# Kernel optimization log

Hardware: AMD Instinct MI355X
Metric: run time of the kernel (lower is better)

Reference implementation:

```python
import jax, jax.numpy as jnp
import numpy as np
from jax import lax

BN_EPS = 1e-5

def _conv1d_same(x, w):
    # x: [N, 1, C], w: [1, 1, k] with k odd -> SAME padding along channel axis
    k = w.shape[-1]
    return lax.conv_general_dilated(x, w, window_strides=(1,),
                                    padding=[(k // 2, k // 2)],
                                    dimension_numbers=('NCH', 'OIH', 'NCH'))

def setup_inputs() -> dict:
    key = jax.random.key(0)
    ks = jax.random.split(key, 6)
    B, C, H, W = 4, 64, 64, 64
    kk = 3  # kernel size from in_dim=64: t=int(abs(log2(64)+1)/2)=3 (odd)
    x = jax.random.normal(ks[0], (B, C, H, W), dtype=jnp.float32)
    q_w = jax.random.normal(ks[1], (1, 1, kk), dtype=jnp.float32) * 0.5
    k_w = jax.random.normal(ks[2], (1, 1, kk), dtype=jnp.float32) * 0.5
    v_w = jax.random.normal(ks[3], (C, C), dtype=jnp.float32) * (1.0 / np.sqrt(C))
    v_b = jnp.zeros((C,), dtype=jnp.float32)
    gamma = jax.random.uniform(ks[4], (1,), dtype=jnp.float32, minval=0.5, maxval=1.5)
    bn_w = jnp.ones((C,), dtype=jnp.float32)
    bn_b = jnp.zeros((C,), dtype=jnp.float32)
    return {"x": x, "q_w": q_w, "k_w": k_w, "v_w": v_w, "v_b": v_b,
            "gamma": gamma, "bn_w": bn_w, "bn_b": bn_b}

def reference(x, q_w, k_w, v_w, v_b, gamma, bn_w, bn_b):
    B, C, H, W = x.shape
    N = H * W
    # conv1d Q/K projections over the channel axis, per spatial position
    xp = x.reshape(B, C, N).transpose(0, 2, 1).reshape(B * N, 1, C)
    q = _conv1d_same(xp, q_w).reshape(B, N, C)   # proj_query: [B, HW, C]
    k = _conv1d_same(xp, k_w).reshape(B, N, C)   # proj_key (pre-permute)
    energy = jnp.einsum('bnc,bmc->bnm', q, k)    # [B, HW, HW]
    attn = jax.nn.softmax(energy, axis=-1)
    # 1x1 value conv
    v = jnp.einsum('oc,bchw->bohw', v_w, x) + v_b[None, :, None, None]
    vv = v.reshape(B, C, N)
    # bmm(value, attention^T)
    out = jnp.einsum('bcm,bnm->bcn', vv, attn).reshape(B, C, H, W)
    y = gamma[0] * out
    # BatchNorm2d, training mode (batch statistics, biased variance)
    mean = jnp.mean(y, axis=(0, 2, 3), keepdims=True)
    var = jnp.var(y, axis=(0, 2, 3), keepdims=True)
    y = (y - mean) * lax.rsqrt(var + BN_EPS)
    y = y * bn_w[None, :, None, None] + bn_b[None, :, None, None]
    return y + x
```

## Files before the change

### kernel.cpp

```cpp
#include <hip/hip_runtime.h>
#include <stdint.h>

using f16 = _Float16;

typedef _Float16 f16x8 __attribute__((ext_vector_type(8)));
typedef _Float16 f16x4 __attribute__((ext_vector_type(4)));
typedef float f32x4 __attribute__((ext_vector_type(4)));

#define LOG2E 1.44269504088896340736f

__device__ __forceinline__ f16 f2h(float f) { return (f16)f; }

#if __has_builtin(__builtin_amdgcn_exp2f)
__device__ __forceinline__ float fexp2(float x) { return __builtin_amdgcn_exp2f(x); }
#else
__device__ __forceinline__ float fexp2(float x) { return exp2f(x); }
#endif

typedef __attribute__((address_space(1))) const uint32_t gu32;
typedef __attribute__((address_space(3))) uint32_t lu32;

__device__ __forceinline__ void dma16(const void* g, void* l) {
  __builtin_amdgcn_global_load_lds((gu32*)g, (lu32*)l, 16, 0, 0);
}

__device__ __forceinline__ f16x8 cvt8(const float* p) {
  const float4 a = *(const float4*)p;
  const float4 b = *(const float4*)(p + 4);
  f16x8 r;
  r[0] = (f16)a.x; r[1] = (f16)a.y; r[2] = (f16)a.z; r[3] = (f16)a.w;
  r[4] = (f16)b.x; r[5] = (f16)b.y; r[6] = (f16)b.z; r[7] = (f16)b.w;
  return r;
}


__global__ __launch_bounds__(256, 2) void pam_pre(
    const float* __restrict__ x, const float* __restrict__ qw,
    const float* __restrict__ kw, const float* __restrict__ vw,
    const float* __restrict__ vb,
    f16* __restrict__ qa, f16* __restrict__ ka2, f16* __restrict__ va3,
    float* __restrict__ gz)
{
  __shared__ alignas(16) f16 xt[16 * 72];
  const int tid = threadIdx.x;
  const int b = blockIdx.x >> 8;
  const int n0 = (blockIdx.x & 255) << 4;
  const int lane = tid & 63;
  const int wv = tid >> 6;
  const int quad = lane >> 4, l15 = lane & 15;

  if (blockIdx.x == 0 && tid < 128) gz[tid] = 0.f;

  {
    const int c = tid >> 2;
    const int j0 = (tid & 3) << 2;
    const float4 v0 = *(const float4*)(x + ((size_t)(b * 64 + c) << 12) + n0 + j0);
    xt[(j0 + 0) * 72 + c] = f2h(v0.x);
    xt[(j0 + 1) * 72 + c] = f2h(v0.y);
    xt[(j0 + 2) * 72 + c] = f2h(v0.z);
    xt[(j0 + 3) * 72 + c] = f2h(v0.w);
  }
  __syncthreads();

  if (tid < 128) {
    const float qw0 = qw[0], qw1 = qw[1], qw2 = qw[2];
    const float kw0 = kw[0], kw1 = kw[1], kw2 = kw[2];
    const int n = tid >> 3;
    const int c8 = tid & 7;
    const f16x8 v0 = *(const f16x8*)&xt[n * 72 + c8 * 8];
    const float lm = (c8 > 0) ? (float)xt[n * 72 + c8 * 8 - 1] : 0.f;
    const float rp = (c8 < 7) ? (float)xt[n * 72 + c8 * 8 + 8] : 0.f;
    f16x8 qv8, kv8;
#pragma unroll
    for (int j = 0; j < 8; ++j) {
      const float xm = (j == 0) ? lm : (float)v0[j - 1];
      const float x0 = (float)v0[j];
      const float xp = (j == 7) ? rp : (float)v0[j + 1];
      qv8[j] = f2h((qw0 * xm + qw1 * x0 + qw2 * xp) * LOG2E);
      kv8[j] = f2h(kw0 * xm + kw1 * x0 + kw2 * xp);
    }
    const int nn = n0 + n;
    *(f16x8*)(qa + ((size_t)((b << 12) + nn) << 6) + c8 * 8) = qv8;
    const int np = nn ^ ((((nn >> 3) & 1) << 2) | ((nn >> 4) & 1));
    *(f16x8*)(ka2 + (((size_t)(b * 8 + c8)) << 15) + (np << 3)) = kv8;
  }

  {
    const f16x8 a0 = *(const f16x8*)&xt[l15 * 72 + quad * 8];
    const f16x8 a1 = *(const f16x8*)&xt[l15 * 72 + quad * 8 + 32];
    const int co = wv * 16 + l15;
    const f16x8 b0 = cvt8(vw + co * 64 + quad * 8);
    const f16x8 b1 = cvt8(vw + co * 64 + quad * 8 + 32);
    f32x4 z = {0.f, 0.f, 0.f, 0.f};
    z = __builtin_amdgcn_mfma_f32_16x16x32_f16(a0, b0, z, 0, 0, 0);
    z = __builtin_amdgcn_mfma_f32_16x16x32_f16(a1, b1, z, 0, 0, 0);
    const float vbv = vb[co];
    f16x4 pv;
#pragma unroll
    for (int r = 0; r < 4; ++r) pv[r] = f2h(z[r] + vbv);
    const int nb = n0 + quad * 4;
    *(f16x4*)(va3 + (((size_t)(b * 512 + (nb >> 3))) << 9)
              + (co << 3) + (nb & 7)) = pv;
  }
}

__global__ __launch_bounds__(512, 6) void pam_attn(
    const f16* __restrict__ qa, const f16* __restrict__ ka2,
    const f16* __restrict__ va3, const float* __restrict__ gam,
    float* __restrict__ y0, float* __restrict__ gs1, float* __restrict__ gs2)
{
  __shared__ alignas(16) f16 kbuf[2][8192];
  __shared__ float ldsO[32 * 65];
  __shared__ float ldsM[4][32], ldsL[4][32], ldsMg[32], ldsInv[32];

  const int tid = threadIdx.x;
  const int wv = tid >> 6, lane = tid & 63;
  const int quad = lane >> 4, l15 = lane & 15;
  const int ks = wv & 3, qh = wv >> 2;
  const int b = blockIdx.x & 3;
  const int qb = blockIdx.x >> 2;
  const int qb0 = qb << 5;
  const int phase = qb & 31;

  for (int i = tid; i < 32 * 65; i += 512) ldsO[i] = 0.f;

  const int bn = b << 12;
  f16x8 bq0, bq1;
  {
    const int q = qb0 + qh * 16 + l15;
    const f16* qp = qa + ((size_t)(bn + q) << 6) + quad * 8;
    bq0 = *(const f16x8*)qp;
    bq1 = *(const f16x8*)(qp + 32);
  }

  const f16* kg0 = ka2 + (((size_t)(b * 8 + wv)) << 15) + (lane << 3);
  const f16* vgp = va3 + ((size_t)b << 18) + ((ks * 4 + quad) << 9) + (l15 << 3);

  f32x4 o[4] = {};
  float m = -1e30f, lp = 0.f;

  dma16(kg0 + ((size_t)phase << 10),       kbuf[0] + (wv << 10));
  dma16(kg0 + ((size_t)phase << 10) + 512, kbuf[0] + (wv << 10) + 512);
  __syncthreads();

  const int u = l15 >> 2;
  const int xmsk = ((u & 1) << 2) | (u >> 1);
  const int pos0 = (ks << 5) + (u << 3) + (l15 & 3);
  const int koff0 = (pos0 ^ xmsk) << 3;
  const int koff1 = koff0 ^ 32;

#pragma unroll 1
  for (int kt = 0; kt < 32; ++kt) {
    const int cur = kt & 1;
    const int gcur = (kt + phase) & 31;

    const f16* vt = vgp + ((size_t)gcur << 13);
    const f16x8 av0 = *(const f16x8*)(vt);
    const f16x8 av1 = *(const f16x8*)(vt + 128);
    const f16x8 av2 = *(const f16x8*)(vt + 256);
    const f16x8 av3 = *(const f16x8*)(vt + 384);

    {
      const int tn = (kt + 1 + phase) & 31;
      f16* kd = kbuf[cur ^ 1] + (wv << 10);
      dma16(kg0 + ((size_t)tn << 10),       kd);
      dma16(kg0 + ((size_t)tn << 10) + 512, kd + 512);
    }

    const f16* kc = kbuf[cur];
    const f16x8 ak00 = *(const f16x8*)(kc + (quad << 10) + koff0);
    const f16x8 ak01 = *(const f16x8*)(kc + ((4 + quad) << 10) + koff0);
    const f16x8 ak10 = *(const f16x8*)(kc + (quad << 10) + koff1);
    const f16x8 ak11 = *(const f16x8*)(kc + ((4 + quad) << 10) + koff1);

    f32x4 z0, z1;
    {
      f32x4 z = {0.f, 0.f, 0.f, 0.f};
      z = __builtin_amdgcn_mfma_f32_16x16x32_f16(ak00, bq0, z, 0, 0, 0);
      z0 = __builtin_amdgcn_mfma_f32_16x16x32_f16(ak01, bq1, z, 0, 0, 0);
    }
    {
      f32x4 z = {0.f, 0.f, 0.f, 0.f};
      z = __builtin_amdgcn_mfma_f32_16x16x32_f16(ak10, bq0, z, 0, 0, 0);
      z1 = __builtin_amdgcn_mfma_f32_16x16x32_f16(ak11, bq1, z, 0, 0, 0);
    }

    float tmax = fmaxf(fmaxf(fmaxf(z0[0], z0[1]), fmaxf(z0[2], z0[3])),
                       fmaxf(fmaxf(z1[0], z1[1]), fmaxf(z1[2], z1[3])));
    tmax = fmaxf(tmax, __shfl_xor(tmax, 16, 64));
    tmax = fmaxf(tmax, __shfl_xor(tmax, 32, 64));
    const bool need = !__all(tmax <= m + 8.f);
    const float mn = need ? fmaxf(m, tmax) : m;

    const float p0 = fexp2(z0[0] - mn);
    const float p1 = fexp2(z0[1] - mn);
    const float p2 = fexp2(z0[2] - mn);
    const float p3 = fexp2(z0[3] - mn);
    const float p4 = fexp2(z1[0] - mn);
    const float p5 = fexp2(z1[1] - mn);
    const float p6 = fexp2(z1[2] - mn);
    const float p7 = fexp2(z1[3] - mn);
    const float ts = ((p0 + p1) + (p2 + p3)) + ((p4 + p5) + (p6 + p7));

    f16x8 pa;
    pa[0] = f2h(p0); pa[1] = f2h(p1); pa[2] = f2h(p2); pa[3] = f2h(p3);
    pa[4] = f2h(p4); pa[5] = f2h(p5); pa[6] = f2h(p6); pa[7] = f2h(p7);

    if (need) {
      const float al = fexp2(m - mn);
      lp = lp * al + ts;
      m = mn;
#pragma unroll
      for (int ct = 0; ct < 4; ++ct)
        for (int r = 0; r < 4; ++r) o[ct][r] *= al;
    } else {
      lp += ts;
    }

    o[0] = __builtin_amdgcn_mfma_f32_16x16x32_f16(av0, pa, o[0], 0, 0, 0);
    o[1] = __builtin_amdgcn_mfma_f32_16x16x32_f16(av1, pa, o[1], 0, 0, 0);
    o[2] = __builtin_amdgcn_mfma_f32_16x16x32_f16(av2, pa, o[2], 0, 0, 0);
    o[3] = __builtin_amdgcn_mfma_f32_16x16x32_f16(av3, pa, o[3], 0, 0, 0);
    __syncthreads();
  }

  {
    float v = lp;
    v += __shfl_xor(v, 16, 64);
    v += __shfl_xor(v, 32, 64);
    if (quad == 0) {
      ldsM[ks][qh * 16 + l15] = m;
      ldsL[ks][qh * 16 + l15] = v;
    }
  }
  __syncthreads();

  if (tid < 32) {
    const float M = fmaxf(fmaxf(ldsM[0][tid], ldsM[1][tid]),
                          fmaxf(ldsM[2][tid], ldsM[3][tid]));
    const float lt = ldsL[0][tid] * fexp2(ldsM[0][tid] - M) +
                     ldsL[1][tid] * fexp2(ldsM[1][tid] - M) +
                     ldsL[2][tid] * fexp2(ldsM[2][tid] - M) +
                     ldsL[3][tid] * fexp2(ldsM[3][tid] - M);
    ldsMg[tid] = M;
    ldsInv[tid] = 1.f / lt;
  }
  __syncthreads();

  {
    const int q = qh * 16 + l15;
    const float sc = fexp2(m - ldsMg[q]);
#pragma unroll
    for (int ct = 0; ct < 4; ++ct)
      for (int r = 0; r < 4; ++r)
        atomicAdd(&ldsO[q * 65 + ct * 16 + quad * 4 + r], o[ct][r] * sc);
  }
  __syncthreads();

  const float g = gam[0];
  {
    const int c = tid >> 3;
    const int q0 = (tid & 7) << 2;
    float4 v4;
    float* vp = &v4.x;
    float s1 = 0.f, s2 = 0.f;
    for (int r = 0; r < 4; ++r) {
      const float val = g * ldsO[(q0 + r) * 65 + c] * ldsInv[q0 + r];
      vp[r] = val; s1 += val; s2 += val * val;
    }
    *(float4*)(y0 + ((size_t)(b * 64 + c) << 12) + qb0 + q0) = v4;
    s1 += __shfl_xor(s1, 1, 64);
    s2 += __shfl_xor(s2, 1, 64);
    s1 += __shfl_xor(s1, 2, 64);
    s2 += __shfl_xor(s2, 2, 64);
    s1 += __shfl_xor(s1, 4, 64);
    s2 += __shfl_xor(s2, 4, 64);
    if ((tid & 7) == 0) {
      atomicAdd(&gs1[c], s1);
      atomicAdd(&gs2[c], s2);
    }
  }
}

__global__ __launch_bounds__(256, 2) void pam_apply(
    const float* __restrict__ y0, const float* __restrict__ x,
    const float* __restrict__ gs1, const float* __restrict__ gs2,
    const float* __restrict__ bnw, const float* __restrict__ bnb,
    float* __restrict__ out)
{
  const int i = (blockIdx.x * 256 + threadIdx.x) << 2;
  const int c = (i >> 12) & 63;
  const float inv_n = 1.f / 16384.f;
  const float mean = gs1[c] * inv_n;
  const float var = fmaxf(gs2[c] * inv_n - mean * mean, 0.f);
  const float sc = bnw[c] * rsqrtf(var + 1e-5f);
  const float sh = bnb[c] - mean * sc;
  const float4 y = *(const float4*)(y0 + i);
  const float4 xv = *(const float4*)(x + i);
  float4 r;
  r.x = y.x * sc + sh + xv.x;
  r.y = y.y * sc + sh + xv.y;
  r.z = y.z * sc + sh + xv.z;
  r.w = y.w * sc + sh + xv.w;
  *(float4*)(out + i) = r;
}

extern "C" void kernel_launch(void* const* d_in, const int* in_sizes, int n_in,
                              void* d_out, int out_size, void* d_ws, size_t ws_size,
                              hipStream_t stream)
{
  (void)in_sizes; (void)n_in; (void)out_size; (void)ws_size;
  const float* x   = (const float*)d_in[0];
  const float* qw  = (const float*)d_in[1];
  const float* kw  = (const float*)d_in[2];
  const float* vw  = (const float*)d_in[3];
  const float* vb  = (const float*)d_in[4];
  const float* gam = (const float*)d_in[5];
  const float* bnw = (const float*)d_in[6];
  const float* bnb = (const float*)d_in[7];

  char* ws = (char*)d_ws;
  f16*   qa  = (f16*)(ws);
  f16*   ka2 = (f16*)(ws + (2u << 20));
  f16*   va3 = (f16*)(ws + (4u << 20));
  float* y0  = (float*)(ws + (6u << 20));
  float* gs1 = (float*)(ws + (10u << 20));
  float* gs2 = (float*)(ws + (10u << 20) + 256);

  pam_pre  <<<1024, 256, 0, stream>>>(x, qw, kw, vw, vb, qa, ka2, va3, gs1);
  pam_attn <<<512, 512, 0, stream>>>(qa, ka2, va3, gam, y0, gs1, gs2);
  pam_apply<<<1024, 256, 0, stream>>>(y0, x, gs1, gs2, bnw, bnb, (float*)d_out);
}
```

Baseline: 147.0 us.

## Fuse projection, attention and BatchNorm apply into one persistent kernel with grid barriers

Merges the pre-projection, attention and BN-apply kernels into one 512-block kernel that uses two atomic-counter grid barriers: one after Q/K/V projection and one after the BN statistics are accumulated. The attention output stays in LDS across the second barrier, so the fp32 y0 intermediate is never written to or read back from global memory. This removes two kernel launches and a global round trip, but a small zeroing kernel is added in front. The grid barrier requires all 512 blocks to be resident at once, which the launch bounds of 2 per CU must guarantee, and the spin-waits can serialize or deadlock if residency fails.

```diff
diff --git a/kernel.cpp b/kernel.cpp
--- a/kernel.cpp
+++ b/kernel.cpp
@@ -34,27 +34,40 @@
 }
 
 
-__global__ __launch_bounds__(256, 2) void pam_pre(
+__global__ __launch_bounds__(256, 1) void pam_zero(float* gz, int* ctr) {
+  if (threadIdx.x < 128) gz[threadIdx.x] = 0.f;
+  if (threadIdx.x < 2) ctr[threadIdx.x] = 0;
+}
+
+__global__ __launch_bounds__(512, 2) void pam_fused(
     const float* __restrict__ x, const float* __restrict__ qw,
     const float* __restrict__ kw, const float* __restrict__ vw,
-    const float* __restrict__ vb,
+    const float* __restrict__ vb, const float* __restrict__ gam,
+    const float* __restrict__ bnw, const float* __restrict__ bnb,
     f16* __restrict__ qa, f16* __restrict__ ka2, f16* __restrict__ va3,
-    float* __restrict__ gz)
+    float* __restrict__ gs1, float* __restrict__ gs2, int* __restrict__ ctr,
+    float* __restrict__ out)
 {
-  __shared__ alignas(16) f16 xt[16 * 72];
+  __shared__ alignas(16) f16 kbuf[2][8192];
+  __shared__ float ldsO[32 * 65];
+  __shared__ float ldsM[4][32], ldsL[4][32], ldsMg[32], ldsInv[32];
+
   const int tid = threadIdx.x;
-  const int b = blockIdx.x >> 8;
-  const int n0 = (blockIdx.x & 255) << 4;
-  const int lane = tid & 63;
-  const int wv = tid >> 6;
+  const int wv = tid >> 6, lane = tid & 63;
   const int quad = lane >> 4, l15 = lane & 15;
-
-  if (blockIdx.x == 0 && tid < 128) gz[tid] = 0.f;
-
-  {
-    const int c = tid >> 2;
-    const int j0 = (tid & 3) << 2;
-    const float4 v0 = *(const float4*)(x + ((size_t)(b * 64 + c) << 12) + n0 + j0);
+  const int ks = wv & 3, qh = wv >> 2;
+  const int b = blockIdx.x & 3;
+  const int qb = blockIdx.x >> 2;
+  const int qb0 = qb << 5;
+  const int phase = qb & 31;
+
+  for (int i = tid; i < 32 * 65; i += 512) ldsO[i] = 0.f;
+
+  f16* const xt = kbuf[0];
+  {
+    const int c = tid >> 3;
+    const int j0 = (tid & 7) << 2;
+    const float4 v0 = *(const float4*)(x + ((size_t)(b * 64 + c) << 12) + qb0 + j0);
     xt[(j0 + 0) * 72 + c] = f2h(v0.x);
     xt[(j0 + 1) * 72 + c] = f2h(v0.y);
     xt[(j0 + 2) * 72 + c] = f2h(v0.z);
@@ -62,7 +75,7 @@
   }
   __syncthreads();
 
-  if (tid < 128) {
+  if (tid < 256) {
     const float qw0 = qw[0], qw1 = qw[1], qw2 = qw[2];
     const float kw0 = kw[0], kw1 = kw[1], kw2 = kw[2];
     const int n = tid >> 3;
@@ -79,16 +92,17 @@
       qv8[j] = f2h((qw0 * xm + qw1 * x0 + qw2 * xp) * LOG2E);
       kv8[j] = f2h(kw0 * xm + kw1 * x0 + kw2 * xp);
     }
-    const int nn = n0 + n;
+    const int nn = qb0 + n;
     *(f16x8*)(qa + ((size_t)((b << 12) + nn) << 6) + c8 * 8) = qv8;
     const int np = nn ^ ((((nn >> 3) & 1) << 2) | ((nn >> 4) & 1));
     *(f16x8*)(ka2 + (((size_t)(b * 8 + c8)) << 15) + (np << 3)) = kv8;
   }
 
   {
-    const f16x8 a0 = *(const f16x8*)&xt[l15 * 72 + quad * 8];
-    const f16x8 a1 = *(const f16x8*)&xt[l15 * 72 + quad * 8 + 32];
-    const int co = wv * 16 + l15;
+    const int nt = wv & 1, cg = wv >> 1;
+    const f16x8 a0 = *(const f16x8*)&xt[(nt * 16 + l15) * 72 + quad * 8];
+    const f16x8 a1 = *(const f16x8*)&xt[(nt * 16 + l15) * 72 + quad * 8 + 32];
+    const int co = cg * 16 + l15;
     const f16x8 b0 = cvt8(vw + co * 64 + quad * 8);
     const f16x8 b1 = cvt8(vw + co * 64 + quad * 8 + 32);
     f32x4 z = {0.f, 0.f, 0.f, 0.f};
@@ -98,31 +112,20 @@
     f16x4 pv;
 #pragma unroll
     for (int r = 0; r < 4; ++r) pv[r] = f2h(z[r] + vbv);
-    const int nb = n0 + quad * 4;
+    const int nb = qb0 + nt * 16 + quad * 4;
     *(f16x4*)(va3 + (((size_t)(b * 512 + (nb >> 3))) << 9)
               + (co << 3) + (nb & 7)) = pv;
   }
-}
-
-__global__ __launch_bounds__(512, 6) void pam_attn(
-    const f16* __restrict__ qa, const f16* __restrict__ ka2,
-    const f16* __restrict__ va3, const float* __restrict__ gam,
-    float* __restrict__ y0, float* __restrict__ gs1, float* __restrict__ gs2)
-{
-  __shared__ alignas(16) f16 kbuf[2][8192];
-  __shared__ float ldsO[32 * 65];
-  __shared__ float ldsM[4][32], ldsL[4][32], ldsMg[32], ldsInv[32];
-
-  const int tid = threadIdx.x;
-  const int wv = tid >> 6, lane = tid & 63;
-  const int quad = lane >> 4, l15 = lane & 15;
-  const int ks = wv & 3, qh = wv >> 2;
-  const int b = blockIdx.x & 3;
-  const int qb = blockIdx.x >> 2;
-  const int qb0 = qb << 5;
-  const int phase = qb & 31;
-
-  for (int i = tid; i < 32 * 65; i += 512) ldsO[i] = 0.f;
+
+  __syncthreads();
+  __threadfence();
+  if (tid == 0) {
+    atomicAdd(ctr, 1);
+    while (__hip_atomic_load(ctr, __ATOMIC_RELAXED, __HIP_MEMORY_SCOPE_AGENT) < 512)
+      __builtin_amdgcn_s_sleep(8);
+  }
+  __syncthreads();
+  __threadfence();
 
   const int bn = b << 12;
   f16x8 bq0, bq1;
@@ -261,14 +264,12 @@
   {
     const int c = tid >> 3;
     const int q0 = (tid & 7) << 2;
-    float4 v4;
-    float* vp = &v4.x;
     float s1 = 0.f, s2 = 0.f;
+#pragma unroll
     for (int r = 0; r < 4; ++r) {
       const float val = g * ldsO[(q0 + r) * 65 + c] * ldsInv[q0 + r];
-      vp[r] = val; s1 += val; s2 += val * val;
-    }
-    *(float4*)(y0 + ((size_t)(b * 64 + c) << 12) + qb0 + q0) = v4;
+      s1 += val; s2 += val * val;
+    }
     s1 += __shfl_xor(s1, 1, 64);
     s2 += __shfl_xor(s2, 1, 64);
     s1 += __shfl_xor(s1, 2, 64);
@@ -280,29 +281,37 @@
       atomicAdd(&gs2[c], s2);
     }
   }
-}
-
-__global__ __launch_bounds__(256, 2) void pam_apply(
-    const float* __restrict__ y0, const float* __restrict__ x,
-    const float* __restrict__ gs1, const float* __restrict__ gs2,
-    const float* __restrict__ bnw, const float* __restrict__ bnb,
-    float* __restrict__ out)
-{
-  const int i = (blockIdx.x * 256 + threadIdx.x) << 2;
-  const int c = (i >> 12) & 63;
-  const float inv_n = 1.f / 16384.f;
-  const float mean = gs1[c] * inv_n;
-  const float var = fmaxf(gs2[c] * inv_n - mean * mean, 0.f);
-  const float sc = bnw[c] * rsqrtf(var + 1e-5f);
-  const float sh = bnb[c] - mean * sc;
-  const float4 y = *(const float4*)(y0 + i);
-  const float4 xv = *(const float4*)(x + i);
-  float4 r;
-  r.x = y.x * sc + sh + xv.x;
-  r.y = y.y * sc + sh + xv.y;
-  r.z = y.z * sc + sh + xv.z;
-  r.w = y.w * sc + sh + xv.w;
-  *(float4*)(out + i) = r;
+
+  __syncthreads();
+  __threadfence();
+  if (tid == 0) {
+    atomicAdd(ctr + 1, 1);
+    while (__hip_atomic_load(ctr + 1, __ATOMIC_RELAXED, __HIP_MEMORY_SCOPE_AGENT) < 512)
+      __builtin_amdgcn_s_sleep(8);
+  }
+  __syncthreads();
+  __threadfence();
+
+  {
+    const int c = tid >> 3;
+    const int q0 = (tid & 7) << 2;
+    const float inv_n = 1.f / 16384.f;
+    const float mean = gs1[c] * inv_n;
+    const float var = fmaxf(gs2[c] * inv_n - mean * mean, 0.f);
+    const float bsc = bnw[c] * rsqrtf(var + 1e-5f);
+    const float bsh = bnb[c] - mean * bsc;
+    const size_t base = ((size_t)(b * 64 + c) << 12) + qb0 + q0;
+    const float4 xv = *(const float4*)(x + base);
+    const float* xp = &xv.x;
+    float4 ov;
+    float* op = &ov.x;
+#pragma unroll
+    for (int r = 0; r < 4; ++r) {
+      const float val = g * ldsO[(q0 + r) * 65 + c] * ldsInv[q0 + r];
+      op[r] = val * bsc + bsh + xp[r];
+    }
+    *(float4*)(out + base) = ov;
+  }
 }
 
 extern "C" void kernel_launch(void* const* d_in, const int* in_sizes, int n_in,
@@ -323,11 +332,11 @@
   f16*   qa  = (f16*)(ws);
   f16*   ka2 = (f16*)(ws + (2u << 20));
   f16*   va3 = (f16*)(ws + (4u << 20));
-  float* y0  = (float*)(ws + (6u << 20));
-  float* gs1 = (float*)(ws + (10u << 20));
-  float* gs2 = (float*)(ws + (10u << 20) + 256);
-
-  pam_pre  <<<1024, 256, 0, stream>>>(x, qw, kw, vw, vb, qa, ka2, va3, gs1);
-  pam_attn <<<512, 512, 0, stream>>>(qa, ka2, va3, gam, y0, gs1, gs2);
-  pam_apply<<<1024, 256, 0, stream>>>(y0, x, gs1, gs2, bnw, bnb, (float*)d_out);
-}
+  float* gs1 = (float*)(ws + (6u << 20));
+  float* gs2 = (float*)(ws + (6u << 20) + 256);
+  int*   ctr = (int*)(ws + (6u << 20) + 512);
+
+  pam_zero <<<1, 256, 0, stream>>>(gs1, ctr);
+  pam_fused<<<512, 512, 0, stream>>>(x, qw, kw, vw, vb, gam, bnw, bnb,
+                                     qa, ka2, va3, gs1, gs2, ctr, (float*)d_out);
+}
```

Result: slower. 412.5 us (+180.5%).

## Give each wave private K tile buffers and drop per-iteration block barrier

Applied to the files above, without the earlier changes.

Each wave now DMA-loads its own copy of the K tiles it needs into a private double-buffered LDS region, so the per-iteration __syncthreads is replaced by an explicit vmcnt wait. The K layout swizzle in the projection kernel is removed and the per-wave gather mapping replaces it. This trades four times the LDS for K (and lower occupancy, launch bounds 6 to 4) and duplicated K loads across waves for the removal of block-wide synchronization every tile. The prefetch is also moved after the QK MFMAs.

```diff
diff --git a/kernel.cpp b/kernel.cpp
--- a/kernel.cpp
+++ b/kernel.cpp
@@ -81,8 +81,7 @@
     }
     const int nn = n0 + n;
     *(f16x8*)(qa + ((size_t)((b << 12) + nn) << 6) + c8 * 8) = qv8;
-    const int np = nn ^ ((((nn >> 3) & 1) << 2) | ((nn >> 4) & 1));
-    *(f16x8*)(ka2 + (((size_t)(b * 8 + c8)) << 15) + (np << 3)) = kv8;
+    *(f16x8*)(ka2 + (((size_t)(b * 8 + c8)) << 15) + (nn << 3)) = kv8;
   }
 
   {
@@ -104,12 +103,12 @@
   }
 }
 
-__global__ __launch_bounds__(512, 6) void pam_attn(
+__global__ __launch_bounds__(512, 4) void pam_attn(
     const f16* __restrict__ qa, const f16* __restrict__ ka2,
     const f16* __restrict__ va3, const float* __restrict__ gam,
     float* __restrict__ y0, float* __restrict__ gs1, float* __restrict__ gs2)
 {
-  __shared__ alignas(16) f16 kbuf[2][8192];
+  __shared__ alignas(16) f16 kbuf[8][4096];
   __shared__ float ldsO[32 * 65];
   __shared__ float ldsM[4][32], ldsL[4][32], ldsMg[32], ldsInv[32];
 
@@ -123,6 +122,7 @@
   const int phase = qb & 31;
 
   for (int i = tid; i < 32 * 65; i += 512) ldsO[i] = 0.f;
+  __syncthreads();
 
   const int bn = b << 12;
   f16x8 bq0, bq1;
@@ -133,21 +133,26 @@
     bq1 = *(const f16x8*)(qp + 32);
   }
 
-  const f16* kg0 = ka2 + (((size_t)(b * 8 + wv)) << 15) + (lane << 3);
+  const int s31 = lane & 31;
+  const int kmap = (((s31 & 15) >> 2) << 3) + (s31 & 3) + ((s31 >> 4) << 2);
+  const f16* kgs = ka2 + (((size_t)(b * 8 + (lane >> 5))) << 15)
+                 + ((ks * 32 + kmap) << 3);
+  f16* const kwv = kbuf[wv];
+
   const f16* vgp = va3 + ((size_t)b << 18) + ((ks * 4 + quad) << 9) + (l15 << 3);
 
   f32x4 o[4] = {};
   float m = -1e30f, lp = 0.f;
 
-  dma16(kg0 + ((size_t)phase << 10),       kbuf[0] + (wv << 10));
-  dma16(kg0 + ((size_t)phase << 10) + 512, kbuf[0] + (wv << 10) + 512);
-  __syncthreads();
-
-  const int u = l15 >> 2;
-  const int xmsk = ((u & 1) << 2) | (u >> 1);
-  const int pos0 = (ks << 5) + (u << 3) + (l15 & 3);
-  const int koff0 = (pos0 ^ xmsk) << 3;
-  const int koff1 = koff0 ^ 32;
+  const int koff = ((quad >> 1) << 9) + ((quad & 1) << 8) + (l15 << 3);
+
+  {
+    const f16* src = kgs + ((size_t)phase << 10);
+    dma16(src,          kwv);
+    dma16(src + 65536,  kwv + 512);
+    dma16(src + 131072, kwv + 1024);
+    dma16(src + 196608, kwv + 1536);
+  }
 
 #pragma unroll 1
   for (int kt = 0; kt < 32; ++kt) {
@@ -159,19 +164,16 @@
     const f16x8 av1 = *(const f16x8*)(vt + 128);
     const f16x8 av2 = *(const f16x8*)(vt + 256);
     const f16x8 av3 = *(const f16x8*)(vt + 384);
-
-    {
-      const int tn = (kt + 1 + phase) & 31;
-      f16* kd = kbuf[cur ^ 1] + (wv << 10);
-      dma16(kg0 + ((size_t)tn << 10),       kd);
-      dma16(kg0 + ((size_t)tn << 10) + 512, kd + 512);
-    }
-
-    const f16* kc = kbuf[cur];
-    const f16x8 ak00 = *(const f16x8*)(kc + (quad << 10) + koff0);
-    const f16x8 ak01 = *(const f16x8*)(kc + ((4 + quad) << 10) + koff0);
-    const f16x8 ak10 = *(const f16x8*)(kc + (quad << 10) + koff1);
-    const f16x8 ak11 = *(const f16x8*)(kc + ((4 + quad) << 10) + koff1);
+    __builtin_amdgcn_sched_barrier(0);
+
+    asm volatile("s_waitcnt vmcnt(4)" ::: "memory");
+    __builtin_amdgcn_sched_barrier(0);
+
+    const f16* kc = kwv + (cur << 11);
+    const f16x8 ak00 = *(const f16x8*)(kc + koff);
+    const f16x8 ak01 = *(const f16x8*)(kc + koff + 1024);
+    const f16x8 ak10 = *(const f16x8*)(kc + koff + 128);
+    const f16x8 ak11 = *(const f16x8*)(kc + koff + 1152);
 
     f32x4 z0, z1;
     {
@@ -183,6 +185,16 @@
       f32x4 z = {0.f, 0.f, 0.f, 0.f};
       z = __builtin_amdgcn_mfma_f32_16x16x32_f16(ak10, bq0, z, 0, 0, 0);
       z1 = __builtin_amdgcn_mfma_f32_16x16x32_f16(ak11, bq1, z, 0, 0, 0);
+    }
+
+    if (kt < 31) {
+      const int tn = (kt + 1 + phase) & 31;
+      const f16* src = kgs + ((size_t)tn << 10);
+      f16* dst = kwv + ((cur ^ 1) << 11);
+      dma16(src,          dst);
+      dma16(src + 65536,  dst + 512);
+      dma16(src + 131072, dst + 1024);
+      dma16(src + 196608, dst + 1536);
     }
 
     float tmax = fmaxf(fmaxf(fmaxf(z0[0], z0[1]), fmaxf(z0[2], z0[3])),
@@ -221,8 +233,9 @@
     o[1] = __builtin_amdgcn_mfma_f32_16x16x32_f16(av1, pa, o[1], 0, 0, 0);
     o[2] = __builtin_amdgcn_mfma_f32_16x16x32_f16(av2, pa, o[2], 0, 0, 0);
     o[3] = __builtin_amdgcn_mfma_f32_16x16x32_f16(av3, pa, o[3], 0, 0, 0);
-    __syncthreads();
-  }
+  }
+
+  asm volatile("s_waitcnt vmcnt(0)" ::: "memory");
 
   {
     float v = lp;
```

Measured after the change: 150.4 us. 1.02x slower.
